# Optimization experiments

Measured on AMD Instinct MI355X. Metric: run time of the kernel, lower is better.

## Reference

```python
import jax, jax.numpy as jnp
import numpy as np

N_NODES = 100000
N_EDGES = 1600000
IN_F = 128
HID_F = 128
N_CLS = 40


def _linear_params(key, out_f, in_f):
    k1, k2 = jax.random.split(key)
    s = 1.0 / np.sqrt(in_f)
    w = jax.random.uniform(k1, (out_f, in_f), jnp.float32, -s, s)
    b = jax.random.uniform(k2, (out_f,), jnp.float32, -s, s)
    return w, b


def setup_inputs() -> dict:
    key = jax.random.key(0)
    ks = jax.random.split(key, 9)
    in_feat = jax.random.normal(ks[0], (N_NODES, IN_F), jnp.float32)
    src = jax.random.randint(ks[1], (N_EDGES,), 0, N_NODES, jnp.int32)
    dst = jax.random.randint(ks[2], (N_EDGES,), 0, N_NODES, jnp.int32)
    pool_w1, pool_b1 = _linear_params(ks[3], IN_F, IN_F)
    self_w1, self_b1 = _linear_params(ks[4], HID_F, IN_F)
    neigh_w1, neigh_b1 = _linear_params(ks[5], HID_F, IN_F)
    pool_w2, pool_b2 = _linear_params(ks[6], HID_F, HID_F)
    self_w2, self_b2 = _linear_params(ks[7], N_CLS, HID_F)
    neigh_w2, neigh_b2 = _linear_params(ks[8], N_CLS, HID_F)
    return dict(in_feat=in_feat, src=src, dst=dst,
                pool_w1=pool_w1, pool_b1=pool_b1, self_w1=self_w1, self_b1=self_b1,
                neigh_w1=neigh_w1, neigh_b1=neigh_b1,
                pool_w2=pool_w2, pool_b2=pool_b2, self_w2=self_w2, self_b2=self_b2,
                neigh_w2=neigh_w2, neigh_b2=neigh_b2)


def sage_conv_pool(h, src, dst, pool_w, pool_b, self_w, self_b, neigh_w, neigh_b):
    # fc_pool + relu on nodes first (N < E), then gather per edge
    m = jax.nn.relu(h @ pool_w.T + pool_b)            # [N, d]
    msgs = m[src]                                     # [E, d] gather
    agg = jax.ops.segment_max(msgs, dst, num_segments=N_NODES)  # [N, d]
    agg = jnp.where(jnp.isfinite(agg), agg, 0.0)      # zero for isolated nodes
    return h @ self_w.T + self_b + agg @ neigh_w.T + neigh_b


def reference(in_feat, src, dst,
              pool_w1, pool_b1, self_w1, self_b1, neigh_w1, neigh_b1,
              pool_w2, pool_b2, self_w2, self_b2, neigh_w2, neigh_b2):
    h = sage_conv_pool(in_feat, src, dst, pool_w1, pool_b1, self_w1, self_b1, neigh_w1, neigh_b1)
    h = jax.nn.relu(h)  # dropout is identity in eval mode
    h = sage_conv_pool(h, src, dst, pool_w2, pool_b2, self_w2, self_b2, neigh_w2, neigh_b2)
    return h
```

## Files before the change

### kernel.cpp

```cpp
#include <hip/hip_runtime.h>


#define N_FEAT 128
#define NWG_A 256
#define BSHIFT 10
#define NBMAX 128

typedef __attribute__((ext_vector_type(8))) short bf16x8;
typedef __attribute__((ext_vector_type(4))) float f32x4;

static __device__ __forceinline__ unsigned short f2bf(float f) {
    unsigned u = __float_as_uint(f);
    unsigned r = (u + 0x7fffu + ((u >> 16) & 1u)) >> 16;
    return (unsigned short)r;
}

__global__ void prep_kernel(const float* __restrict__ pw1, const float* __restrict__ sw1,
                            const float* __restrict__ nw1, const float* __restrict__ pw2,
                            const float* __restrict__ sw2, const float* __restrict__ nw2,
                            const float* __restrict__ sb1, const float* __restrict__ nb1,
                            const float* __restrict__ sb2, const float* __restrict__ nb2,
                            unsigned short* __restrict__ wb_p1, unsigned short* __restrict__ wb_s1,
                            unsigned short* __restrict__ wb_n1, unsigned short* __restrict__ wb_p2,
                            unsigned short* __restrict__ wb_s2, unsigned short* __restrict__ wb_n2,
                            float* __restrict__ b_sn1, float* __restrict__ b_sn2)
{
    int t = blockIdx.x * 256 + threadIdx.x;
    if (t < 16384) {
        wb_p1[t] = f2bf(pw1[t]);
        wb_s1[t] = f2bf(sw1[t]);
        wb_n1[t] = f2bf(nw1[t]);
        wb_p2[t] = f2bf(pw2[t]);
    }
    if (t < 6144) {
        int row = t >> 7;
        wb_s2[t] = (row < 40) ? f2bf(sw2[t]) : 0;
        wb_n2[t] = (row < 40) ? f2bf(nw2[t]) : 0;
    }
    if (t < 128) b_sn1[t] = sb1[t] + nb1[t];
    if (t < 64)  b_sn2[t] = (t < 40) ? (sb2[t] + nb2[t]) : 0.f;
}

__global__ void f2b_kernel(const float4* __restrict__ in, ushort4* __restrict__ out, int n)
{
    int i = blockIdx.x * 256 + threadIdx.x;
    if (i < n) {
        float4 v = in[i];
        ushort4 o;
        o.x = f2bf(v.x); o.y = f2bf(v.y); o.z = f2bf(v.z); o.w = f2bf(v.w);
        out[i] = o;
    }
}


__global__ __launch_bounds__(256) void bin_count_kernel(const int* __restrict__ dst,
                                                        int* __restrict__ wgcnt,
                                                        int E, int NB)
{
    __shared__ int cnt[NBMAX];
    const int wg = blockIdx.x, tid = threadIdx.x;
    if (tid < NB) cnt[tid] = 0;
    __syncthreads();
    const int slab = (E + NWG_A - 1) / NWG_A;
    const int e0 = wg * slab;
    const int e1 = min(e0 + slab, E);
    for (int e = e0 + tid; e < e1; e += 256)
        atomicAdd(&cnt[dst[e] >> BSHIFT], 1);
    __syncthreads();
    if (tid < NB) wgcnt[tid * NWG_A + wg] = cnt[tid];
}

__global__ __launch_bounds__(256) void bin_scan_kernel(const int* __restrict__ wgcnt,
                                                       int* __restrict__ binoff, int NB)
{
    __shared__ int sh[256];
    const int t = threadIdx.x;
    const int base = t * NB;
    int s = 0;
    for (int k = 0; k < NB; k++) s += wgcnt[base + k];
    sh[t] = s;
    __syncthreads();
    for (int off = 1; off < 256; off <<= 1) {
        int x = (t >= off) ? sh[t - off] : 0;
        __syncthreads();
        sh[t] += x;
        __syncthreads();
    }
    int run = sh[t] - s;
    for (int k = 0; k < NB; k++) {
        int v = wgcnt[base + k];
        binoff[base + k] = run;
        run += v;
    }
    if (t == 255) binoff[NB * NWG_A] = run;
}

__global__ __launch_bounds__(256) void bin_scatter_kernel(const int* __restrict__ src,
                                                          const int* __restrict__ dst,
                                                          const int* __restrict__ binoff,
                                                          unsigned* __restrict__ binned,
                                                          int E, int NB)
{
    __shared__ int cur[NBMAX];
    const int wg = blockIdx.x, tid = threadIdx.x;
    if (tid < NB) cur[tid] = binoff[tid * NWG_A + wg];
    __syncthreads();
    const int slab = (E + NWG_A - 1) / NWG_A;
    const int e0 = wg * slab;
    const int e1 = min(e0 + slab, E);
    for (int e = e0 + tid; e < e1; e += 256) {
        int d = dst[e];
        int b = d >> BSHIFT;
        unsigned rec = ((unsigned)(d & ((1 << BSHIFT) - 1)) << 17) | (unsigned)src[e];
        int p = atomicAdd(&cur[b], 1);
        binned[p] = rec;
    }
}

__global__ __launch_bounds__(256) void csr_build_kernel(const unsigned* __restrict__ binned,
                                                        const int* __restrict__ binoff,
                                                        int* __restrict__ csr,
                                                        int* __restrict__ offsets,
                                                        int* __restrict__ counts, int M)
{
    __shared__ int cnt[1 << BSHIFT];
    __shared__ int scn[1 << BSHIFT];
    __shared__ int sh[256];
    const int b = blockIdx.x, t = threadIdx.x;
    const int rs = binoff[b * NWG_A];
    const int re = binoff[(b + 1) * NWG_A];

    for (int j = t; j < (1 << BSHIFT); j += 256) cnt[j] = 0;
    __syncthreads();
    for (int i = rs + t; i < re; i += 256)
        atomicAdd(&cnt[binned[i] >> 17], 1);
    __syncthreads();

    const int base4 = t * 4;
    int v[4];
#pragma unroll
    for (int k = 0; k < 4; k++) v[k] = cnt[base4 + k];
    int s = v[0] + v[1] + v[2] + v[3];
    sh[t] = s;
    __syncthreads();
    for (int off = 1; off < 256; off <<= 1) {
        int x = (t >= off) ? sh[t - off] : 0;
        __syncthreads();
        sh[t] += x;
        __syncthreads();
    }
    int run = sh[t] - s;
#pragma unroll
    for (int k = 0; k < 4; k++) {
        scn[base4 + k] = run;
        run += v[k];
    }

    const int node0 = b << BSHIFT;
#pragma unroll
    for (int k = 0; k < 4; k++) {
        int j = base4 + k;
        int node = node0 + j;
        if (node < M) {
            counts[node] = v[k];
            offsets[node] = rs + scn[j];
        }
    }
    __syncthreads();

    for (int i = rs + t; i < re; i += 256) {
        unsigned r = binned[i];
        int p = atomicAdd(&scn[r >> 17], 1);
        csr[rs + p] = (int)(r & 0x1FFFFu);
    }
}

__global__ __launch_bounds__(256) void gather_max_kernel(
    const unsigned* __restrict__ m4, const int* __restrict__ csr,
    const int* __restrict__ offsets, const int* __restrict__ counts,
    unsigned* __restrict__ agg4, int Nn)
{
    int wid = (blockIdx.x * 256 + threadIdx.x) >> 6;
    int lane = threadIdx.x & 63;
    if (wid >= Nn) return;
    int start = offsets[wid];
    int deg = counts[wid];
    unsigned lo = 0, hi = 0;
    for (int j0 = 0; j0 < deg; j0 += 64) {
        int nb = deg - j0;
        if (nb > 64) nb = 64;
        int sl = csr[start + j0 + (lane < nb ? lane : nb - 1)];
        int j = 0;
        for (; j + 4 <= nb; j += 4) {
            int s0 = __shfl(sl, j + 0), s1 = __shfl(sl, j + 1);
            int s2 = __shfl(sl, j + 2), s3 = __shfl(sl, j + 3);
            unsigned v0 = m4[(size_t)s0 * 64 + lane];
            unsigned v1 = m4[(size_t)s1 * 64 + lane];
            unsigned v2 = m4[(size_t)s2 * 64 + lane];
            unsigned v3 = m4[(size_t)s3 * 64 + lane];
            unsigned a = v0 & 0xffffu, b = v0 & 0xffff0000u;
            unsigned c = v1 & 0xffffu, d = v1 & 0xffff0000u;
            a = a > (v2 & 0xffffu) ? a : (v2 & 0xffffu);
            b = b > (v2 & 0xffff0000u) ? b : (v2 & 0xffff0000u);
            c = c > (v3 & 0xffffu) ? c : (v3 & 0xffffu);
            d = d > (v3 & 0xffff0000u) ? d : (v3 & 0xffff0000u);
            a = a > c ? a : c;
            b = b > d ? b : d;
            lo = lo > a ? lo : a;
            hi = hi > b ? hi : b;
        }
        for (; j < nb; j++) {
            int s = __shfl(sl, j);
            unsigned v = m4[(size_t)s * 64 + lane];
            unsigned a = v & 0xffffu, b = v & 0xffff0000u;
            lo = lo > a ? lo : a;
            hi = hi > b ? hi : b;
        }
    }
    agg4[(size_t)wid * 64 + lane] = lo | hi;
}

template<int NT, bool RELU, int NPAIRS, bool F32OUT>
__global__ __launch_bounds__(256, 2) void mfma_gemm_kernel(
    const unsigned short* __restrict__ A0, const unsigned short* __restrict__ B0,
    const unsigned short* __restrict__ A1, const unsigned short* __restrict__ B1,
    const float* __restrict__ bias, void* __restrict__ Cout, int M, int Nout)
{
    constexpr int NR = NT * 16;
    __shared__ unsigned short As[128 * 136];
    __shared__ unsigned short Bs[NR * 136];
    __shared__ float BsF[NR];

    const int tid = threadIdx.x;
    const int w = tid >> 6, lane = tid & 63;
    const int q = lane >> 4, r16 = lane & 15;
    const int m0 = blockIdx.x * 128;

    if (tid < NR) BsF[tid] = (tid < Nout) ? bias[tid] : 0.f;

    f32x4 acc[2][NT];
#pragma unroll
    for (int i = 0; i < 2; i++)
#pragma unroll
        for (int j = 0; j < NT; j++) acc[i][j] = (f32x4){0.f, 0.f, 0.f, 0.f};

    for (int p = 0; p < NPAIRS; p++) {
        const unsigned short* __restrict__ A = p ? A1 : A0;
        const unsigned short* __restrict__ B = p ? B1 : B0;
        if (p) __syncthreads();
#pragma unroll
        for (int i = 0; i < 8; i++) {
            int j = tid + i * 256;
            int row = j >> 4, c = j & 15;
            int grow = m0 + row; if (grow >= M) grow = M - 1;
            uint4 v = *(const uint4*)&A[(size_t)grow * 128 + c * 8];
            *(uint4*)&As[row * 136 + c * 8] = v;
        }
        for (int j = tid; j < NR * 16; j += 256) {
            int row = j >> 4, c = j & 15;
            uint4 v = *(const uint4*)&B[(size_t)row * 128 + c * 8];
            *(uint4*)&Bs[row * 136 + c * 8] = v;
        }
        __syncthreads();

#pragma unroll
        for (int k0 = 0; k0 < 128; k0 += 32) {
            bf16x8 af[2];
#pragma unroll
            for (int rt = 0; rt < 2; rt++)
                af[rt] = *(const bf16x8*)&As[(w * 32 + rt * 16 + r16) * 136 + k0 + q * 8];
#pragma unroll
            for (int ct = 0; ct < NT; ct++) {
                bf16x8 bfr = *(const bf16x8*)&Bs[(ct * 16 + r16) * 136 + k0 + q * 8];
#pragma unroll
                for (int rt = 0; rt < 2; rt++)
                    acc[rt][ct] = __builtin_amdgcn_mfma_f32_16x16x32_bf16(
                        af[rt], bfr, acc[rt][ct], 0, 0, 0);
            }
        }
    }

#pragma unroll
    for (int rt = 0; rt < 2; rt++) {
#pragma unroll
        for (int ct = 0; ct < NT; ct++) {
            int col = ct * 16 + r16;
#pragma unroll
            for (int r = 0; r < 4; r++) {
                int grow = m0 + w * 32 + rt * 16 + q * 4 + r;
                float v = acc[rt][ct][r] + BsF[col];
                if (RELU) v = fmaxf(v, 0.f);
                if (grow < M && col < Nout) {
                    if (F32OUT)
                        ((float*)Cout)[(size_t)grow * Nout + col] = v;
                    else
                        ((unsigned short*)Cout)[(size_t)grow * Nout + col] = f2bf(v);
                }
            }
        }
    }
}

extern "C" void kernel_launch(void* const* d_in, const int* in_sizes, int n_in,
                              void* d_out, int out_size, void* d_ws, size_t ws_size,
                              hipStream_t stream)
{
    const float* in_feat = (const float*)d_in[0];
    const int*   src     = (const int*)d_in[1];
    const int*   dst     = (const int*)d_in[2];
    const float* pw1 = (const float*)d_in[3];  const float* pb1 = (const float*)d_in[4];
    const float* sw1 = (const float*)d_in[5];  const float* sb1 = (const float*)d_in[6];
    const float* nw1 = (const float*)d_in[7];  const float* nb1 = (const float*)d_in[8];
    const float* pw2 = (const float*)d_in[9];  const float* pb2 = (const float*)d_in[10];
    const float* sw2 = (const float*)d_in[11]; const float* sb2 = (const float*)d_in[12];
    const float* nw2 = (const float*)d_in[13]; const float* nb2 = (const float*)d_in[14];
    float* out = (float*)d_out;

    const int M = in_sizes[0] / N_FEAT;
    const int E = in_sizes[1];
    const int NB = (M + (1 << BSHIFT) - 1) >> BSHIFT;

    char* base = (char*)d_ws;
    size_t off = 0;
    auto alloc = [&](size_t bytes) { char* p = base + off; off = (off + bytes + 255) & ~(size_t)255; return p; };
    unsigned short* wb_p1 = (unsigned short*)alloc(16384 * 2);
    unsigned short* wb_s1 = (unsigned short*)alloc(16384 * 2);
    unsigned short* wb_n1 = (unsigned short*)alloc(16384 * 2);
    unsigned short* wb_p2 = (unsigned short*)alloc(16384 * 2);
    unsigned short* wb_s2 = (unsigned short*)alloc(6144 * 2);
    unsigned short* wb_n2 = (unsigned short*)alloc(6144 * 2);
    float* b_sn1 = (float*)alloc(128 * 4);
    float* b_sn2 = (float*)alloc(64 * 4);
    unsigned short* in_b = (unsigned short*)alloc((size_t)M * 128 * 2);
    unsigned short* mb   = (unsigned short*)alloc((size_t)M * 128 * 2);
    unsigned short* agg  = (unsigned short*)alloc((size_t)M * 128 * 2);
    unsigned short* h1   = (unsigned short*)alloc((size_t)M * 128 * 2);
    int* counts  = (int*)alloc((size_t)M * 4);
    int* offsets = (int*)alloc((size_t)M * 4);
    int* wgcnt   = (int*)alloc((size_t)NB * NWG_A * 4);
    int* binoff  = (int*)alloc(((size_t)NB * NWG_A + 1) * 4);
    unsigned* binned = (unsigned*)alloc((size_t)E * 4);
    int* csr     = (int*)alloc((size_t)E * 4);

    const int gemm_grid = (M + 127) / 128;
    const int gather_grid = (M * 64 + 255) / 256;
    const int nf4 = M * 128 / 4;

    prep_kernel<<<64, 256, 0, stream>>>(pw1, sw1, nw1, pw2, sw2, nw2,
                                        sb1, nb1, sb2, nb2,
                                        wb_p1, wb_s1, wb_n1, wb_p2, wb_s2, wb_n2,
                                        b_sn1, b_sn2);
    f2b_kernel<<<(nf4 + 255) / 256, 256, 0, stream>>>((const float4*)in_feat, (ushort4*)in_b, nf4);

    bin_count_kernel<<<NWG_A, 256, 0, stream>>>(dst, wgcnt, E, NB);
    bin_scan_kernel<<<1, 256, 0, stream>>>(wgcnt, binoff, NB);
    bin_scatter_kernel<<<NWG_A, 256, 0, stream>>>(src, dst, binoff, binned, E, NB);
    csr_build_kernel<<<NB, 256, 0, stream>>>(binned, binoff, csr, offsets, counts, M);

    mfma_gemm_kernel<8, true, 1, false><<<gemm_grid, 256, 0, stream>>>(
        in_b, wb_p1, nullptr, nullptr, pb1, mb, M, 128);
    gather_max_kernel<<<gather_grid, 256, 0, stream>>>(
        (const unsigned*)mb, csr, offsets, counts, (unsigned*)agg, M);
    mfma_gemm_kernel<8, true, 2, false><<<gemm_grid, 256, 0, stream>>>(
        in_b, wb_s1, agg, wb_n1, b_sn1, h1, M, 128);

    mfma_gemm_kernel<8, true, 1, false><<<gemm_grid, 256, 0, stream>>>(
        h1, wb_p2, nullptr, nullptr, pb2, mb, M, 128);
    gather_max_kernel<<<gather_grid, 256, 0, stream>>>(
        (const unsigned*)mb, csr, offsets, counts, (unsigned*)agg, M);
    mfma_gemm_kernel<3, false, 2, true><<<gemm_grid, 256, 0, stream>>>(
        h1, wb_s2, agg, wb_n2, b_sn2, out, M, 40);
}
```

Baseline: 432.1 us.

## Vectorize gather-max to 16-byte loads and stream GEMM A operand from global

The gather-max kernel now has each wavefront process four neighbor rows at once. Each lane loads 16 bytes (8 bf16) with a packed elementwise unsigned max, and the four groups are combined with cross-lane xor shuffles. The GEMM kernel drops the LDS staging of the A tile and reads A fragments directly from global memory into MFMA registers. That frees shared memory so launch bounds can allow 4 workgroups per CU. The trade-offs are uncoalesced per-lane A reads in the GEMM, possible redundant clamped loads for degree tails, and extra shuffle-reduction work.

```diff
diff --git a/kernel.cpp b/kernel.cpp
--- a/kernel.cpp
+++ b/kernel.cpp
@@ -7,6 +7,7 @@
 #define NBMAX 128
 
 typedef __attribute__((ext_vector_type(8))) short bf16x8;
+typedef __attribute__((ext_vector_type(8))) unsigned short u16x8;
 typedef __attribute__((ext_vector_type(4))) float f32x4;
 
 static __device__ __forceinline__ unsigned short f2bf(float f) {
@@ -52,7 +53,6 @@
     }
 }
 
-
 __global__ __launch_bounds__(256) void bin_count_kernel(const int* __restrict__ dst,
                                                         int* __restrict__ wgcnt,
                                                         int E, int NB)
@@ -176,58 +176,49 @@
 }
 
 __global__ __launch_bounds__(256) void gather_max_kernel(
-    const unsigned* __restrict__ m4, const int* __restrict__ csr,
+    const u16x8* __restrict__ m16, const int* __restrict__ csr,
     const int* __restrict__ offsets, const int* __restrict__ counts,
-    unsigned* __restrict__ agg4, int Nn)
+    u16x8* __restrict__ agg16, int Nn)
 {
     int wid = (blockIdx.x * 256 + threadIdx.x) >> 6;
     int lane = threadIdx.x & 63;
     if (wid >= Nn) return;
+    const int g = lane >> 4, c = lane & 15;
     int start = offsets[wid];
     int deg = counts[wid];
-    unsigned lo = 0, hi = 0;
+    u16x8 acc = (u16x8){0, 0, 0, 0, 0, 0, 0, 0};
     for (int j0 = 0; j0 < deg; j0 += 64) {
         int nb = deg - j0;
         if (nb > 64) nb = 64;
         int sl = csr[start + j0 + (lane < nb ? lane : nb - 1)];
-        int j = 0;
-        for (; j + 4 <= nb; j += 4) {
-            int s0 = __shfl(sl, j + 0), s1 = __shfl(sl, j + 1);
-            int s2 = __shfl(sl, j + 2), s3 = __shfl(sl, j + 3);
-            unsigned v0 = m4[(size_t)s0 * 64 + lane];
-            unsigned v1 = m4[(size_t)s1 * 64 + lane];
-            unsigned v2 = m4[(size_t)s2 * 64 + lane];
-            unsigned v3 = m4[(size_t)s3 * 64 + lane];
-            unsigned a = v0 & 0xffffu, b = v0 & 0xffff0000u;
-            unsigned c = v1 & 0xffffu, d = v1 & 0xffff0000u;
-            a = a > (v2 & 0xffffu) ? a : (v2 & 0xffffu);
-            b = b > (v2 & 0xffff0000u) ? b : (v2 & 0xffff0000u);
-            c = c > (v3 & 0xffffu) ? c : (v3 & 0xffffu);
-            d = d > (v3 & 0xffff0000u) ? d : (v3 & 0xffff0000u);
-            a = a > c ? a : c;
-            b = b > d ? b : d;
-            lo = lo > a ? lo : a;
-            hi = hi > b ? hi : b;
-        }
-        for (; j < nb; j++) {
-            int s = __shfl(sl, j);
-            unsigned v = m4[(size_t)s * 64 + lane];
-            unsigned a = v & 0xffffu, b = v & 0xffff0000u;
-            lo = lo > a ? lo : a;
-            hi = hi > b ? hi : b;
-        }
-    }
-    agg4[(size_t)wid * 64 + lane] = lo | hi;
+        for (int j = 0; j < nb; j += 4) {
+            int jj = j + g;
+            if (jj >= nb) jj = nb - 1;
+            int s = __shfl(sl, jj);
+            u16x8 v = m16[(size_t)s * 16 + c];
+            acc = __builtin_elementwise_max(acc, v);
+        }
+    }
+#pragma unroll
+    for (int d = 16; d <= 32; d <<= 1) {
+        int4 a = *(int4*)&acc;
+        int4 t;
+        t.x = __shfl_xor(a.x, d);
+        t.y = __shfl_xor(a.y, d);
+        t.z = __shfl_xor(a.z, d);
+        t.w = __shfl_xor(a.w, d);
+        acc = __builtin_elementwise_max(acc, *(u16x8*)&t);
+    }
+    if (g == 0) agg16[(size_t)wid * 16 + c] = acc;
 }
 
 template<int NT, bool RELU, int NPAIRS, bool F32OUT>
-__global__ __launch_bounds__(256, 2) void mfma_gemm_kernel(
+__global__ __launch_bounds__(256, 4) void mfma_gemm_kernel(
     const unsigned short* __restrict__ A0, const unsigned short* __restrict__ B0,
     const unsigned short* __restrict__ A1, const unsigned short* __restrict__ B1,
     const float* __restrict__ bias, void* __restrict__ Cout, int M, int Nout)
 {
     constexpr int NR = NT * 16;
-    __shared__ unsigned short As[128 * 136];
     __shared__ unsigned short Bs[NR * 136];
     __shared__ float BsF[NR];
 
@@ -238,6 +229,13 @@
 
     if (tid < NR) BsF[tid] = (tid < Nout) ? bias[tid] : 0.f;
 
+    int rowA[2];
+#pragma unroll
+    for (int rt = 0; rt < 2; rt++) {
+        int r = m0 + w * 32 + rt * 16 + r16;
+        rowA[rt] = r < M ? r : (M - 1);
+    }
+
     f32x4 acc[2][NT];
 #pragma unroll
     for (int i = 0; i < 2; i++)
@@ -248,18 +246,10 @@
         const unsigned short* __restrict__ A = p ? A1 : A0;
         const unsigned short* __restrict__ B = p ? B1 : B0;
         if (p) __syncthreads();
-#pragma unroll
-        for (int i = 0; i < 8; i++) {
-            int j = tid + i * 256;
-            int row = j >> 4, c = j & 15;
-            int grow = m0 + row; if (grow >= M) grow = M - 1;
-            uint4 v = *(const uint4*)&A[(size_t)grow * 128 + c * 8];
-            *(uint4*)&As[row * 136 + c * 8] = v;
-        }
         for (int j = tid; j < NR * 16; j += 256) {
-            int row = j >> 4, c = j & 15;
-            uint4 v = *(const uint4*)&B[(size_t)row * 128 + c * 8];
-            *(uint4*)&Bs[row * 136 + c * 8] = v;
+            int row = j >> 4, cc = j & 15;
+            uint4 v = *(const uint4*)&B[(size_t)row * 128 + cc * 8];
+            *(uint4*)&Bs[row * 136 + cc * 8] = v;
         }
         __syncthreads();
 
@@ -268,7 +258,7 @@
             bf16x8 af[2];
 #pragma unroll
             for (int rt = 0; rt < 2; rt++)
-                af[rt] = *(const bf16x8*)&As[(w * 32 + rt * 16 + r16) * 136 + k0 + q * 8];
+                af[rt] = *(const bf16x8*)&A[(size_t)rowA[rt] * 128 + k0 + q * 8];
 #pragma unroll
             for (int ct = 0; ct < NT; ct++) {
                 bf16x8 bfr = *(const bf16x8*)&Bs[(ct * 16 + r16) * 136 + k0 + q * 8];
@@ -360,14 +350,14 @@
     mfma_gemm_kernel<8, true, 1, false><<<gemm_grid, 256, 0, stream>>>(
         in_b, wb_p1, nullptr, nullptr, pb1, mb, M, 128);
     gather_max_kernel<<<gather_grid, 256, 0, stream>>>(
-        (const unsigned*)mb, csr, offsets, counts, (unsigned*)agg, M);
+        (const u16x8*)mb, csr, offsets, counts, (u16x8*)agg, M);
     mfma_gemm_kernel<8, true, 2, false><<<gemm_grid, 256, 0, stream>>>(
         in_b, wb_s1, agg, wb_n1, b_sn1, h1, M, 128);
 
     mfma_gemm_kernel<8, true, 1, false><<<gemm_grid, 256, 0, stream>>>(
         h1, wb_p2, nullptr, nullptr, pb2, mb, M, 128);
     gather_max_kernel<<<gather_grid, 256, 0, stream>>>(
-        (const unsigned*)mb, csr, offsets, counts, (unsigned*)agg, M);
+        (const u16x8*)mb, csr, offsets, counts, (u16x8*)agg, M);
     mfma_gemm_kernel<3, false, 2, true><<<gemm_grid, 256, 0, stream>>>(
         h1, wb_s2, agg, wb_n2, b_sn2, out, M, 40);
 }
```

After: 412.7 us. -4.5%, faster.
